# Kernel tuning notes

Measured on AMD Instinct MI355X. Metric: run time of the kernel, lower is better.

## Reference

```python
import jax, jax.numpy as jnp
import numpy as np

N_NODES = 100000
N_EDGES = 1600000
IN_FEATS = 64
OUT_FEATS = 128
N_STEPS = 3


def setup_inputs() -> dict:
    key = jax.random.key(0)
    ks = jax.random.split(key, 9)
    features = jax.random.normal(ks[0], (N_NODES, IN_FEATS), dtype=jnp.float32)
    src = jax.random.randint(ks[1], (N_EDGES,), 0, N_NODES)
    dst = jax.random.randint(ks[2], (N_EDGES,), 0, N_NODES)
    # edge linear (xavier-normal-ish scale)
    s_lin = (2.0 / (OUT_FEATS + OUT_FEATS)) ** 0.5 * (2.0 ** 0.5)
    W = jax.random.normal(ks[3], (OUT_FEATS, OUT_FEATS), dtype=jnp.float32) * s_lin
    b = jnp.zeros((OUT_FEATS,), dtype=jnp.float32)
    # GRUCell params (uniform(-1/sqrt(h), 1/sqrt(h)) as in torch)
    s = 1.0 / (OUT_FEATS ** 0.5)
    W_ih = jax.random.uniform(ks[4], (3 * OUT_FEATS, OUT_FEATS), minval=-s, maxval=s, dtype=jnp.float32)
    W_hh = jax.random.uniform(ks[5], (3 * OUT_FEATS, OUT_FEATS), minval=-s, maxval=s, dtype=jnp.float32)
    b_ih = jax.random.uniform(ks[6], (3 * OUT_FEATS,), minval=-s, maxval=s, dtype=jnp.float32)
    b_hh = jax.random.uniform(ks[7], (3 * OUT_FEATS,), minval=-s, maxval=s, dtype=jnp.float32)
    return {"features": features, "W": W, "b": b, "W_ih": W_ih, "W_hh": W_hh,
            "b_ih": b_ih, "b_hh": b_hh, "src": src, "dst": dst}


def _gru_cell(x, h, W_ih, W_hh, b_ih, b_hh):
    gi = x @ W_ih.T + b_ih   # [N, 3H]
    gh = h @ W_hh.T + b_hh   # [N, 3H]
    i_r, i_z, i_n = jnp.split(gi, 3, axis=-1)
    h_r, h_z, h_n = jnp.split(gh, 3, axis=-1)
    r = jax.nn.sigmoid(i_r + h_r)
    z = jax.nn.sigmoid(i_z + h_z)
    n = jnp.tanh(i_n + r * h_n)
    return (1.0 - z) * n + z * h


def reference(features, W, b, W_ih, W_hh, b_ih, b_hh, src, dst):
    n_nodes = features.shape[0]
    # zero-pad features up to out_feats
    h = jnp.pad(features, ((0, 0), (0, OUT_FEATS - features.shape[1])))
    for _ in range(N_STEPS):
        m = h[src] @ W.T + b                                   # gather + per-edge linear [E, H]
        a = jax.ops.segment_sum(m, dst, num_segments=n_nodes)  # scatter-sum [N, H]
        h = _gru_cell(a, h, W_ih, W_hh, b_ih, b_hh)
    return h
```

## Files before the change

kernel.cpp:

```cpp
#include <hip/hip_runtime.h>
#include <math.h>

#define N_NODES 100000
#define N_EDGES 1600000
#define CSTRIDE 48
#define NGRP 8
#define NODES_PER_GRP ((N_NODES + NGRP - 1) / NGRP)

typedef __attribute__((ext_vector_type(8))) short short8;
typedef __attribute__((ext_vector_type(4))) float f32x4;

__device__ inline unsigned short f32_to_bf16(float x) {
    unsigned u = __float_as_uint(x);
    unsigned r = u + 0x7fff + ((u >> 16) & 1);
    return (unsigned short)(r >> 16);
}
__device__ inline float bf16_to_f32(unsigned short u) {
    return __uint_as_float(((unsigned)u) << 16);
}
__device__ inline void split1(float x, unsigned short& hi, unsigned short& lo) {
    hi = f32_to_bf16(x);
    lo = f32_to_bf16(x - bf16_to_f32(hi));
}
__device__ inline float fast_tanh(float x) {
    float ax = fabsf(x);
    float e  = __expf(2.f * ax);
    float t  = 1.f - 2.f / (e + 1.f);
    return copysignf(t, x);
}

__device__ inline size_t pack_idx(int g, int k) {
    int gate = g >> 7, c = g & 127;
    int w = c >> 4, l15 = c & 15;
    int k0 = k >> 5, r = k & 31, hi8 = r >> 3, j = r & 7;
    int lane = hi8 * 16 + l15;
    return ((size_t)(((w * 3 + gate) * 4 + k0) * 64 + lane)) * 8 + j;
}

__global__ __launch_bounds__(128) void pack_wc_kernel(const float* __restrict__ W_ih,
                                                      const float* __restrict__ W,
                                                      unsigned short* __restrict__ Wcpk) {
    int g = blockIdx.x;
    int k = threadIdx.x;
    float acc = 0.f;
    for (int j = 0; j < 128; ++j)
        acc += W_ih[g * 128 + j] * W[j * 128 + k];
    Wcpk[pack_idx(g, k)] = f32_to_bf16(acc);
}

__global__ __launch_bounds__(256) void pack_whh_kernel(const float* __restrict__ W_hh,
                                                       unsigned short* __restrict__ Whpk) {
    int i = blockIdx.x * 256 + threadIdx.x;
    if (i >= 384 * 128) return;
    Whpk[pack_idx(i >> 7, i & 127)] = f32_to_bf16(W_hh[i]);
}

__global__ __launch_bounds__(384) void bc_kernel(const float* __restrict__ W_ih,
                                                 const float* __restrict__ b,
                                                 float* __restrict__ bc) {
    int g = threadIdx.x;
    if (g >= 384) return;
    float acc = 0.f;
    for (int j = 0; j < 128; ++j)
        acc += W_ih[g * 128 + j] * b[j];
    bc[g] = acc;
}

__global__ __launch_bounds__(256) void init_h_kernel(const float* __restrict__ f,
                                                     unsigned short* __restrict__ h_hi,
                                                     unsigned short* __restrict__ h_lo) {
    int idx = blockIdx.x * 256 + threadIdx.x;
    if (idx >= N_NODES * 32) return;
    int r = idx >> 5, c4 = idx & 31;
    float4 v = make_float4(0.f, 0.f, 0.f, 0.f);
    if (c4 < 16) v = ((const float4*)f)[r * 16 + c4];
    ushort4 hv, lv;
    split1(v.x, hv.x, lv.x); split1(v.y, hv.y, lv.y);
    split1(v.z, hv.z, lv.z); split1(v.w, hv.w, lv.w);
    ((ushort4*)h_hi)[idx] = hv;
    ((ushort4*)h_lo)[idx] = lv;
}

__global__ __launch_bounds__(256) void finalize_kernel(const unsigned short* __restrict__ h_hi,
                                                       const unsigned short* __restrict__ h_lo,
                                                       float* __restrict__ out) {
    int idx = blockIdx.x * 256 + threadIdx.x;
    if (idx >= N_NODES * 32) return;
    ushort4 hv = ((const ushort4*)h_hi)[idx];
    ushort4 lv = ((const ushort4*)h_lo)[idx];
    float4 o;
    o.x = bf16_to_f32(hv.x) + bf16_to_f32(lv.x);
    o.y = bf16_to_f32(hv.y) + bf16_to_f32(lv.y);
    o.z = bf16_to_f32(hv.z) + bf16_to_f32(lv.z);
    o.w = bf16_to_f32(hv.w) + bf16_to_f32(lv.w);
    ((float4*)out)[idx] = o;
}

__global__ __launch_bounds__(256) void fill_xcd_kernel(const int* __restrict__ src,
                                                       const int* __restrict__ dst,
                                                       int* __restrict__ cnt,
                                                       int* __restrict__ csr_src) {
    const int grp  = blockIdx.x & (NGRP - 1);
    const int bing = blockIdx.x / NGRP;
    const int nbg  = gridDim.x / NGRP;
    const int lo   = grp * NODES_PER_GRP;
    const int hi   = lo + NODES_PER_GRP;
    for (int e = bing * 256 + threadIdx.x; e < N_EDGES; e += nbg * 256) {
        int d = __builtin_nontemporal_load(dst + e);
        if (d >= lo && d < hi) {
            int s = __builtin_nontemporal_load(src + e);
            int pos = atomicAdd(&cnt[d], 1);
            if (pos < CSTRIDE) csr_src[(size_t)d * CSTRIDE + pos] = s;
        }
    }
}

__global__ __launch_bounds__(256) void gather_kernel(const unsigned int* __restrict__ hhu,
                                                     const int* __restrict__ cnt,
                                                     const int* __restrict__ csr_src,
                                                     unsigned short* __restrict__ s_hi,
                                                     unsigned short* __restrict__ s_lo) {
    int node = blockIdx.x * 4 + (threadIdx.x >> 6);
    int lane = threadIdx.x & 63;
    int deg = cnt[node];
    int end = (deg < CSTRIDE) ? deg : CSTRIDE;
    const int* lst = csr_src + (size_t)node * CSTRIDE;
    float a0 = 0.f, a1 = 0.f;
    int i = 0;
    for (; i + 7 < end; i += 8) {
        unsigned u[8];
#pragma unroll
        for (int j = 0; j < 8; ++j)
            u[j] = hhu[(size_t)lst[i + j] * 64 + lane];
#pragma unroll
        for (int j = 0; j < 8; ++j) {
            a0 += __uint_as_float(u[j] << 16);
            a1 += __uint_as_float(u[j] & 0xffff0000u);
        }
    }
    if (i + 3 < end) {
        unsigned u[4];
#pragma unroll
        for (int j = 0; j < 4; ++j)
            u[j] = hhu[(size_t)lst[i + j] * 64 + lane];
#pragma unroll
        for (int j = 0; j < 4; ++j) {
            a0 += __uint_as_float(u[j] << 16);
            a1 += __uint_as_float(u[j] & 0xffff0000u);
        }
        i += 4;
    }
    for (; i < end; ++i) {
        unsigned u0 = hhu[(size_t)lst[i] * 64 + lane];
        a0 += __uint_as_float(u0 << 16);
        a1 += __uint_as_float(u0 & 0xffff0000u);
    }
    unsigned short h0, l0, h1, l1;
    split1(a0, h0, l0);
    split1(a1, h1, l1);
    ((ushort2*)s_hi)[(size_t)node * 64 + lane] = (ushort2){h0, h1};
    ((ushort2*)s_lo)[(size_t)node * 64 + lane] = (ushort2){l0, l1};
}

__global__ __launch_bounds__(512, 1) void gru_ps_kernel(
        const unsigned short* __restrict__ s_hi,
        const unsigned short* __restrict__ s_lo,
        const unsigned short* __restrict__ hin_hi,
        const unsigned short* __restrict__ hin_lo,
        unsigned short* __restrict__ hout_hi,
        unsigned short* __restrict__ hout_lo,
        const unsigned short* __restrict__ Wcpk,
        const unsigned short* __restrict__ Whpk,
        const float* __restrict__ bc,
        const float* __restrict__ b_ih,
        const float* __restrict__ b_hh,
        const int* __restrict__ cnt) {
    __shared__ unsigned short lwc[24576];
    __shared__ unsigned short lwh[24576];

    const int tid  = threadIdx.x;
    const int lane = tid & 63;
    const int wv   = tid >> 6;
    const int w4   = wv & 3;
    const int nt   = wv >> 2;
    const int l15  = lane & 15, hi8 = lane >> 4;
    const int ch   = blockIdx.x & 1;
    const int c    = ch * 64 + w4 * 16 + l15;

    {
        const ushort4* gC = (const ushort4*)(Wcpk + (size_t)ch * 24576);
        const ushort4* gH = (const ushort4*)(Whpk + (size_t)ch * 24576);
        ushort4* dC = (ushort4*)lwc;
        ushort4* dH = (ushort4*)lwh;
#pragma unroll
        for (int i = 0; i < 12; ++i) {
            dC[tid + 512 * i] = gC[tid + 512 * i];
            dH[tid + 512 * i] = gH[tid + 512 * i];
        }
    }
    __syncthreads();

    const float bcr = bc[c],   bcz = bc[128 + c],   bcn = bc[256 + c];
    const float bir = b_ih[c], biz = b_ih[128 + c], bin = b_ih[256 + c];
    const float bhr = b_hh[c], bhz = b_hh[128 + c], bhn = b_hh[256 + c];

    for (int tile = blockIdx.x >> 1; tile < N_NODES / 32; tile += gridDim.x >> 1) {
        const int n0 = tile * 32 + nt * 16;

        short8 sh[4], sl[4], hh[4];
#pragma unroll
        for (int k0 = 0; k0 < 4; ++k0) {
            size_t ro = (size_t)(n0 + l15) * 128 + k0 * 32 + hi8 * 8;
            sh[k0] = *(const short8*)&s_hi[ro];
            sl[k0] = *(const short8*)&s_lo[ro];
            hh[k0] = *(const short8*)&hin_hi[ro];
        }
        float hold[4], dg[4];
#pragma unroll
        for (int r = 0; r < 4; ++r) {
            int row = n0 + hi8 * 4 + r;
            size_t gidx = (size_t)row * 128 + c;
            hold[r] = bf16_to_f32(hin_hi[gidx]) + bf16_to_f32(hin_lo[gidx]);
            dg[r]   = (float)cnt[row];
        }

        f32x4 z1[3], z2[3];
#pragma unroll
        for (int g = 0; g < 3; ++g) {
            z1[g] = (f32x4){0.f, 0.f, 0.f, 0.f};
            z2[g] = (f32x4){0.f, 0.f, 0.f, 0.f};
        }
#pragma unroll
        for (int k0 = 0; k0 < 4; ++k0)
#pragma unroll
            for (int g = 0; g < 3; ++g) {
                int fo = (((w4 * 3 + g) * 4 + k0) * 64 + lane) * 8;
                short8 wc = *(const short8*)&lwc[fo];
                short8 wh = *(const short8*)&lwh[fo];
                z1[g] = __builtin_amdgcn_mfma_f32_16x16x32_bf16(sh[k0], wc, z1[g], 0, 0, 0);
                z1[g] = __builtin_amdgcn_mfma_f32_16x16x32_bf16(sl[k0], wc, z1[g], 0, 0, 0);
                z2[g] = __builtin_amdgcn_mfma_f32_16x16x32_bf16(hh[k0], wh, z2[g], 0, 0, 0);
            }

#pragma unroll
        for (int r = 0; r < 4; ++r) {
            int row = n0 + hi8 * 4 + r;
            size_t gidx = (size_t)row * 128 + c;
            float d = dg[r];
            float rr = 1.f / (1.f + __expf(-(z1[0][r] + d * bcr + bir + z2[0][r] + bhr)));
            float zz = 1.f / (1.f + __expf(-(z1[1][r] + d * bcz + biz + z2[1][r] + bhz)));
            float nn_ = fast_tanh(z1[2][r] + d * bcn + bin + rr * (z2[2][r] + bhn));
            float hn = (1.f - zz) * nn_ + zz * hold[r];
            unsigned short shh, sll;
            split1(hn, shh, sll);
            hout_hi[gidx] = shh;
            hout_lo[gidx] = sll;
        }
    }
}

extern "C" void kernel_launch(void* const* d_in, const int* in_sizes, int n_in,
                              void* d_out, int out_size, void* d_ws, size_t ws_size,
                              hipStream_t stream) {
    const float* feat = (const float*)d_in[0];
    const float* W    = (const float*)d_in[1];
    const float* b    = (const float*)d_in[2];
    const float* W_ih = (const float*)d_in[3];
    const float* W_hh = (const float*)d_in[4];
    const float* b_ih = (const float*)d_in[5];
    const float* b_hh = (const float*)d_in[6];
    const int*   src  = (const int*)d_in[7];
    const int*   dst  = (const int*)d_in[8];

    unsigned short* s_hi = (unsigned short*)d_out;
    unsigned short* s_lo = s_hi + (size_t)N_NODES * 128;

    char* w = (char*)d_ws;
    unsigned short* hA_hi = (unsigned short*)w; w += (size_t)N_NODES * 128 * 2;
    unsigned short* hA_lo = (unsigned short*)w; w += (size_t)N_NODES * 128 * 2;
    unsigned short* hB_hi = (unsigned short*)w; w += (size_t)N_NODES * 128 * 2;
    unsigned short* hB_lo = (unsigned short*)w; w += (size_t)N_NODES * 128 * 2;
    unsigned short* Wcpk  = (unsigned short*)w; w += (size_t)384 * 128 * 2;
    unsigned short* Whpk  = (unsigned short*)w; w += (size_t)384 * 128 * 2;
    float*          bc    = (float*)w;          w += 384 * 4;
    int*            cnt   = (int*)w;            w += (size_t)N_NODES * 4;
    int*            csr_src = (int*)w;          w += (size_t)N_NODES * CSTRIDE * 4;

    const int elem_blocks = (N_NODES * 32 + 255) / 256;
    const int gath_blocks = N_NODES / 4;

    init_h_kernel<<<elem_blocks, 256, 0, stream>>>(feat, hA_hi, hA_lo);
    pack_wc_kernel<<<384, 128, 0, stream>>>(W_ih, W, Wcpk);
    pack_whh_kernel<<<(384 * 128 + 255) / 256, 256, 0, stream>>>(W_hh, Whpk);
    bc_kernel<<<1, 384, 0, stream>>>(W_ih, b, bc);

    hipMemsetAsync(cnt, 0, (size_t)N_NODES * 4, stream);
    fill_xcd_kernel<<<1024, 256, 0, stream>>>(src, dst, cnt, csr_src);

    unsigned short* hi_in[3]  = {hA_hi, hB_hi, hA_hi};
    unsigned short* lo_in[3]  = {hA_lo, hB_lo, hA_lo};
    unsigned short* hi_out[3] = {hB_hi, hA_hi, hB_hi};
    unsigned short* lo_out[3] = {hB_lo, hA_lo, hB_lo};
    for (int s = 0; s < 3; ++s) {
        gather_kernel<<<gath_blocks, 256, 0, stream>>>((const unsigned int*)hi_in[s],
                                                       cnt, csr_src, s_hi, s_lo);
        gru_ps_kernel<<<512, 512, 0, stream>>>(s_hi, s_lo,
                                               hi_in[s], lo_in[s],
                                               hi_out[s], lo_out[s],
                                               Wcpk, Whpk, bc, b_ih, b_hh, cnt);
    }
    finalize_kernel<<<elem_blocks, 256, 0, stream>>>(hB_hi, hB_lo, (float*)d_out);
}
```

Baseline: 610.6 us.

## Prefetch GRU activation tiles via double-buffered LDS and batch gather index loads

The GRU kernel now keeps the packed weight fragments in registers and stages each 32-node activation tile through a swizzled, double-buffered LDS buffer. The next tile's global loads are issued while the current tile computes, and the MFMA operands are read from LDS instead of strided global loads. The gather kernel loads all neighbour indices up front with int4 loads and issues up to 48 row loads before accumulating, to expose more memory-level parallelism. The cost is heavy register pressure (96 weight registers, plus 48-entry index and value arrays with a launch-bounds hint) and an extra __syncthreads per tile.

```diff
diff --git a/kernel.cpp b/kernel.cpp
--- a/kernel.cpp
+++ b/kernel.cpp
@@ -6,6 +6,7 @@
 #define CSTRIDE 48
 #define NGRP 8
 #define NODES_PER_GRP ((N_NODES + NGRP - 1) / NGRP)
+#define GRU_NT (N_NODES / 32)
 
 typedef __attribute__((ext_vector_type(8))) short short8;
 typedef __attribute__((ext_vector_type(4))) float f32x4;
@@ -115,42 +116,49 @@
     }
 }
 
-__global__ __launch_bounds__(256) void gather_kernel(const unsigned int* __restrict__ hhu,
-                                                     const int* __restrict__ cnt,
-                                                     const int* __restrict__ csr_src,
-                                                     unsigned short* __restrict__ s_hi,
-                                                     unsigned short* __restrict__ s_lo) {
+__global__ __launch_bounds__(256, 2) void gather_kernel(const unsigned int* __restrict__ hhu,
+                                                        const int* __restrict__ cnt,
+                                                        const int* __restrict__ csr_src,
+                                                        unsigned short* __restrict__ s_hi,
+                                                        unsigned short* __restrict__ s_lo) {
     int node = blockIdx.x * 4 + (threadIdx.x >> 6);
     int lane = threadIdx.x & 63;
     int deg = cnt[node];
     int end = (deg < CSTRIDE) ? deg : CSTRIDE;
     const int* lst = csr_src + (size_t)node * CSTRIDE;
+    const int nb = end & ~7;
+
+    int li[48];
+#pragma unroll
+    for (int base = 0; base < 48; base += 8) {
+        if (base < nb) {
+            int4 p0 = *(const int4*)&lst[base];
+            int4 p1 = *(const int4*)&lst[base + 4];
+            li[base + 0] = p0.x; li[base + 1] = p0.y; li[base + 2] = p0.z; li[base + 3] = p0.w;
+            li[base + 4] = p1.x; li[base + 5] = p1.y; li[base + 6] = p1.z; li[base + 7] = p1.w;
+        }
+    }
+    unsigned u[48];
+#pragma unroll
+    for (int base = 0; base < 48; base += 8) {
+        if (base < nb) {
+#pragma unroll
+            for (int j = 0; j < 8; ++j)
+                u[base + j] = hhu[(size_t)li[base + j] * 64 + lane];
+        }
+    }
     float a0 = 0.f, a1 = 0.f;
-    int i = 0;
-    for (; i + 7 < end; i += 8) {
-        unsigned u[8];
-#pragma unroll
-        for (int j = 0; j < 8; ++j)
-            u[j] = hhu[(size_t)lst[i + j] * 64 + lane];
-#pragma unroll
-        for (int j = 0; j < 8; ++j) {
-            a0 += __uint_as_float(u[j] << 16);
-            a1 += __uint_as_float(u[j] & 0xffff0000u);
-        }
-    }
-    if (i + 3 < end) {
-        unsigned u[4];
-#pragma unroll
-        for (int j = 0; j < 4; ++j)
-            u[j] = hhu[(size_t)lst[i + j] * 64 + lane];
-#pragma unroll
-        for (int j = 0; j < 4; ++j) {
-            a0 += __uint_as_float(u[j] << 16);
-            a1 += __uint_as_float(u[j] & 0xffff0000u);
-        }
-        i += 4;
-    }
-    for (; i < end; ++i) {
+#pragma unroll
+    for (int base = 0; base < 48; base += 8) {
+        if (base < nb) {
+#pragma unroll
+            for (int j = 0; j < 8; ++j) {
+                a0 += __uint_as_float(u[base + j] << 16);
+                a1 += __uint_as_float(u[base + j] & 0xffff0000u);
+            }
+        }
+    }
+    for (int i = nb; i < end; ++i) {
         unsigned u0 = hhu[(size_t)lst[i] * 64 + lane];
         a0 += __uint_as_float(u0 << 16);
         a1 += __uint_as_float(u0 & 0xffff0000u);
@@ -162,7 +170,7 @@
     ((ushort2*)s_lo)[(size_t)node * 64 + lane] = (ushort2){l0, l1};
 }
 
-__global__ __launch_bounds__(512, 1) void gru_ps_kernel(
+__global__ __launch_bounds__(512, 1) void gru_ps2_kernel(
         const unsigned short* __restrict__ s_hi,
         const unsigned short* __restrict__ s_lo,
         const unsigned short* __restrict__ hin_hi,
@@ -177,6 +185,7 @@
         const int* __restrict__ cnt) {
     __shared__ unsigned short lwc[24576];
     __shared__ unsigned short lwh[24576];
+    __shared__ unsigned short abuf[2][3][4096];
 
     const int tid  = threadIdx.x;
     const int lane = tid & 63;
@@ -200,21 +209,51 @@
     }
     __syncthreads();
 
+    short8 wcr[3][4], whr[3][4];
+#pragma unroll
+    for (int g = 0; g < 3; ++g)
+#pragma unroll
+        for (int k0 = 0; k0 < 4; ++k0) {
+            int fo = (((w4 * 3 + g) * 4 + k0) * 64 + lane) * 8;
+            wcr[g][k0] = *(const short8*)&lwc[fo];
+            whr[g][k0] = *(const short8*)&lwh[fo];
+        }
+
     const float bcr = bc[c],   bcz = bc[128 + c],   bcn = bc[256 + c];
     const float bir = b_ih[c], biz = b_ih[128 + c], bin = b_ih[256 + c];
     const float bhr = b_hh[c], bhz = b_hh[128 + c], bhn = b_hh[256 + c];
 
-    for (int tile = blockIdx.x >> 1; tile < N_NODES / 32; tile += gridDim.x >> 1) {
+    const int o  = tid * 16;
+    const int os = o ^ (((o >> 8) & 7) << 4);
+    const int arow = nt * 16 + l15;
+    const int asw  = (arow & 7) << 4;
+
+    const int tstep = gridDim.x >> 1;
+    int tile = blockIdx.x >> 1;
+
+    short8 rs, rl, rh;
+    if (tile < GRU_NT) {
+        size_t gb = (size_t)tile * 32 * 256 + o;
+        rs = *(const short8*)((const char*)s_hi  + gb);
+        rl = *(const short8*)((const char*)s_lo  + gb);
+        rh = *(const short8*)((const char*)hin_hi + gb);
+    }
+    int pb = 0;
+    for (; tile < GRU_NT; tile += tstep) {
+        *(short8*)((char*)abuf[pb][0] + os) = rs;
+        *(short8*)((char*)abuf[pb][1] + os) = rl;
+        *(short8*)((char*)abuf[pb][2] + os) = rh;
+        __syncthreads();
+
+        int ntile = tile + tstep;
+        if (ntile < GRU_NT) {
+            size_t gb = (size_t)ntile * 32 * 256 + o;
+            rs = *(const short8*)((const char*)s_hi  + gb);
+            rl = *(const short8*)((const char*)s_lo  + gb);
+            rh = *(const short8*)((const char*)hin_hi + gb);
+        }
+
         const int n0 = tile * 32 + nt * 16;
-
-        short8 sh[4], sl[4], hh[4];
-#pragma unroll
-        for (int k0 = 0; k0 < 4; ++k0) {
-            size_t ro = (size_t)(n0 + l15) * 128 + k0 * 32 + hi8 * 8;
-            sh[k0] = *(const short8*)&s_hi[ro];
-            sl[k0] = *(const short8*)&s_lo[ro];
-            hh[k0] = *(const short8*)&hin_hi[ro];
-        }
         float hold[4], dg[4];
 #pragma unroll
         for (int r = 0; r < 4; ++r) {
@@ -231,16 +270,19 @@
             z2[g] = (f32x4){0.f, 0.f, 0.f, 0.f};
         }
 #pragma unroll
-        for (int k0 = 0; k0 < 4; ++k0)
+        for (int k0 = 0; k0 < 4; ++k0) {
+            int pa = arow * 256 + k0 * 64 + hi8 * 16;
+            int ps = pa ^ asw;
+            short8 ash = *(const short8*)((const char*)abuf[pb][0] + ps);
+            short8 asl = *(const short8*)((const char*)abuf[pb][1] + ps);
+            short8 ahh = *(const short8*)((const char*)abuf[pb][2] + ps);
 #pragma unroll
             for (int g = 0; g < 3; ++g) {
-                int fo = (((w4 * 3 + g) * 4 + k0) * 64 + lane) * 8;
-                short8 wc = *(const short8*)&lwc[fo];
-                short8 wh = *(const short8*)&lwh[fo];
-                z1[g] = __builtin_amdgcn_mfma_f32_16x16x32_bf16(sh[k0], wc, z1[g], 0, 0, 0);
-                z1[g] = __builtin_amdgcn_mfma_f32_16x16x32_bf16(sl[k0], wc, z1[g], 0, 0, 0);
-                z2[g] = __builtin_amdgcn_mfma_f32_16x16x32_bf16(hh[k0], wh, z2[g], 0, 0, 0);
+                z1[g] = __builtin_amdgcn_mfma_f32_16x16x32_bf16(ash, wcr[g][k0], z1[g], 0, 0, 0);
+                z1[g] = __builtin_amdgcn_mfma_f32_16x16x32_bf16(asl, wcr[g][k0], z1[g], 0, 0, 0);
+                z2[g] = __builtin_amdgcn_mfma_f32_16x16x32_bf16(ahh, whr[g][k0], z2[g], 0, 0, 0);
             }
+        }
 
 #pragma unroll
         for (int r = 0; r < 4; ++r) {
@@ -256,6 +298,7 @@
             hout_hi[gidx] = shh;
             hout_lo[gidx] = sll;
         }
+        pb ^= 1;
     }
 }
 
@@ -304,10 +347,10 @@
     for (int s = 0; s < 3; ++s) {
         gather_kernel<<<gath_blocks, 256, 0, stream>>>((const unsigned int*)hi_in[s],
                                                        cnt, csr_src, s_hi, s_lo);
-        gru_ps_kernel<<<512, 512, 0, stream>>>(s_hi, s_lo,
-                                               hi_in[s], lo_in[s],
-                                               hi_out[s], lo_out[s],
-                                               Wcpk, Whpk, bc, b_ih, b_hh, cnt);
+        gru_ps2_kernel<<<512, 512, 0, stream>>>(s_hi, s_lo,
+                                                hi_in[s], lo_in[s],
+                                                hi_out[s], lo_out[s],
+                                                Wcpk, Whpk, bc, b_ih, b_hh, cnt);
     }
     finalize_kernel<<<elem_blocks, 256, 0, stream>>>(hB_hi, hB_lo, (float*)d_out);
 }
```

Result: slower. 706.2 us (+15.6%).
